# Performance work log

Hardware: AMD Instinct MI355X
Metric: run time of the kernel (lower is better)

## Reference

```python
import jax, jax.numpy as jnp
import numpy as np

NUM_HEADS = 32
NUM_KV_HEADS = 8
HEAD_DIM = 128
PAGE_SIZE = 16
NUM_PAGES = 512
PAGES_PER_SEQ = 256  # 4096 cached tokens
Q_LEN = 1024
SCALE = 0.08838834764831845  # 1/sqrt(HEAD_DIM)


def setup_inputs() -> dict:
    key = jax.random.key(0)
    k1, k2, k3, k4, k5 = jax.random.split(key, 5)
    q = jax.random.normal(k1, (Q_LEN, NUM_HEADS * HEAD_DIM), dtype=jnp.float32)
    k = jax.random.normal(k2, (Q_LEN, NUM_KV_HEADS * HEAD_DIM), dtype=jnp.float32)
    v = jax.random.normal(k3, (Q_LEN, NUM_KV_HEADS * HEAD_DIM), dtype=jnp.float32)
    # paged KV cache: [num_pages, 2 (k/v), num_kv_heads, page_size, head_dim]
    kv_cache = jax.random.normal(
        k4, (NUM_PAGES, 2, NUM_KV_HEADS, PAGE_SIZE, HEAD_DIM), dtype=jnp.float32)
    block_table = jnp.sort(
        jax.random.randint(k5, (PAGES_PER_SEQ,), 0, NUM_PAGES, dtype=jnp.int32))
    return {"q": q, "k": k, "v": v, "kv_cache": kv_cache,
            "block_table": block_table}


def reference(q, k, v, kv_cache, block_table):
    # reshape flat projections into heads
    q = q.reshape(-1, NUM_HEADS, HEAD_DIM)          # [Tq, H, D]
    k = k.reshape(-1, NUM_KV_HEADS, HEAD_DIM)       # [Tq, Hkv, D]
    v = v.reshape(-1, NUM_KV_HEADS, HEAD_DIM)

    # gather paged KV cache into continuous tensors (all pages full)
    pages = kv_cache[block_table]                   # [P, 2, Hkv, ps, D]
    # per-page [Hkv, ps, D] -> [ps, Hkv, D], then concat along token dim
    past = jnp.transpose(pages, (1, 0, 3, 2, 4))    # [2, P, ps, Hkv, D]
    past = past.reshape(2, -1, NUM_KV_HEADS, HEAD_DIM)
    past_k, past_v = past[0], past[1]               # [Tpast, Hkv, D]

    k_full = jnp.concatenate([past_k, k], axis=0)   # [Tkv, Hkv, D]
    v_full = jnp.concatenate([past_v, v], axis=0)

    # GQA: repeat kv heads to match query heads
    heads_per_kv = NUM_HEADS // NUM_KV_HEADS
    k_full = jnp.repeat(k_full, heads_per_kv, axis=1)  # [Tkv, H, D]
    v_full = jnp.repeat(v_full, heads_per_kv, axis=1)

    qh = jnp.transpose(q, (1, 0, 2))                # [H, Tq, D]
    kh = jnp.transpose(k_full, (1, 0, 2))           # [H, Tkv, D]
    vh = jnp.transpose(v_full, (1, 0, 2))

    scores = jnp.einsum('hqd,hkd->hqk', qh, kh) * SCALE  # [H, Tq, Tkv]

    # prefill causal mask exactly as in the source: triu(ones(q_len, kv_len), 1)
    q_len, kv_len = qh.shape[1], kh.shape[1]
    causal = jnp.triu(jnp.ones((q_len, kv_len), dtype=bool), k=1)
    scores = jnp.where(causal[None, :, :], -jnp.inf, scores)

    attn = jax.nn.softmax(scores.astype(jnp.float32), axis=-1).astype(qh.dtype)
    out = jnp.einsum('hqk,hkd->hqd', attn, vh)      # [H, Tq, D]
    out = jnp.transpose(out, (1, 0, 2)).reshape(-1, NUM_HEADS * HEAD_DIM)
    return out
```

## Files before the change

kernel.cpp:

```cpp
#include <hip/hip_runtime.h>
#include <hip/hip_bf16.h>


#define NUM_HEADS 32
#define HEAD_DIM 128
#define Q_STRIDE 4096
#define SCALE 0.08838834764831845f
#define RESCALE_THR 8.0f
#define KSW_TILE 16384
#define VSW_OFF (2 * 1024 * 1024)

typedef short short8 __attribute__((ext_vector_type(8)));
typedef float f32x4 __attribute__((ext_vector_type(4)));
typedef unsigned short ushort_t;
typedef unsigned int uint_t;

__device__ __forceinline__ ushort_t f2bf(float f) {
    return __builtin_bit_cast(ushort_t, __float2bfloat16(f));
}
__device__ __forceinline__ uint_t pk2(float a, float b) {
    return (uint_t)f2bf(a) | ((uint_t)f2bf(b) << 16);
}

__launch_bounds__(256)
__global__ void prep_kv(const float* __restrict__ kvc,
                        const int* __restrict__ bt,
                        char* __restrict__ wsb)
{
    __shared__ float sVt[64 * 128];
    const int blk = blockIdx.x;
    const int hkv = blk >> 4;
    const int jb  = blk & 15;
    const int tid = threadIdx.x;
    char* kout = wsb + (size_t)(hkv * 16 + jb) * KSW_TILE;
    char* vout = wsb + VSW_OFF + (size_t)(hkv * 16 + jb) * KSW_TILE;

#pragma unroll
    for (int i = 0; i < 4; ++i) {
        const int u = tid + i * 256;
        const int t = u >> 4, c = u & 15;
        const int gtok = jb * 64 + t;
        const int page = bt[gtok >> 4];
        const float* src = kvc + (size_t)page * 32768 + (size_t)hkv * 2048
                         + (gtok & 15) * 128 + c * 8;
        float4 a = *(const float4*)src;
        float4 b = *(const float4*)(src + 4);
        uint4 p;
        p.x = pk2(a.x, a.y); p.y = pk2(a.z, a.w);
        p.z = pk2(b.x, b.y); p.w = pk2(b.z, b.w);
        *(uint4*)(kout + t * 256 + ((c * 16) ^ ((t & 7) << 4))) = p;
    }
#pragma unroll
    for (int i = 0; i < 8; ++i) {
        const int u = tid + i * 256;
        const int t = u >> 5, c4 = u & 31;
        const int gtok = jb * 64 + t;
        const int page = bt[gtok >> 4];
        const float* src = kvc + (size_t)page * 32768 + 16384
                         + (size_t)hkv * 2048 + (gtok & 15) * 128 + c4 * 4;
        *(float4*)(sVt + t * 128 + c4 * 4) = *(const float4*)src;
    }
    __syncthreads();
#pragma unroll
    for (int i = 0; i < 4; ++i) {
        const int u = tid + i * 256;
        const int d = u >> 3, ch = u & 7;
        float v[8];
#pragma unroll
        for (int k = 0; k < 8; ++k) v[k] = sVt[(8 * ch + k) * 128 + d];
        uint4 p;
        p.x = pk2(v[0], v[1]); p.y = pk2(v[2], v[3]);
        p.z = pk2(v[4], v[5]); p.w = pk2(v[6], v[7]);
        *(uint4*)(vout + ((d * 128 + 16 * ch) ^ ((d & 7) << 4))) = p;
    }
}

#define GLL16(G, L) __builtin_amdgcn_global_load_lds(                         \
    (const uint_t __attribute__((address_space(1)))*)(G),                     \
    (uint_t __attribute__((address_space(3)))*)(L), 16, 0, 0)

#define STAGE(JB, KB, VB) {                                                   \
    const char* ks = kvbf + (size_t)(hkv * 16 + (JB)) * KSW_TILE              \
                   + w * 4096 + lane * 16;                                    \
    const char* vs = ks + VSW_OFF;                                            \
    _Pragma("unroll")                                                         \
    for (int i = 0; i < 4; ++i) {                                             \
        GLL16(ks + i * 1024, (KB) + w * 4096 + i * 1024);                     \
        GLL16(vs + i * 1024, (VB) + w * 4096 + i * 1024);                     \
    }                                                                         \
}

__launch_bounds__(256)
__global__ void attn_main(const float* __restrict__ q,
                          const char* __restrict__ kvbf,
                          float* __restrict__ out)
{
    __shared__ __align__(16) char sK[2][16384];
    __shared__ __align__(16) char sV[2][16384];
    __shared__ __align__(16) char sP[4][2048];

    const int bid = blockIdx.x;
    const int h   = bid & 31;
    const int qt  = 15 - (bid >> 5);
    const int hkv = h >> 2;
    const int tid  = threadIdx.x;
    const int w    = tid >> 6;
    const int lane = tid & 63;
    const int l15  = lane & 15;
    const int lhi  = lane >> 4;

    short8 qf[4];
    {
        const int qrow = qt * 64 + w * 16 + l15;
        const float* qp = q + (size_t)qrow * Q_STRIDE + h * HEAD_DIM;
#pragma unroll
        for (int s = 0; s < 4; ++s) {
            const int d0 = s * 32 + lhi * 8;
            float4 a = *(const float4*)(qp + d0);
            float4 b = *(const float4*)(qp + d0 + 4);
            short8 v;
            v[0] = (short)f2bf(a.x * SCALE); v[1] = (short)f2bf(a.y * SCALE);
            v[2] = (short)f2bf(a.z * SCALE); v[3] = (short)f2bf(a.w * SCALE);
            v[4] = (short)f2bf(b.x * SCALE); v[5] = (short)f2bf(b.y * SCALE);
            v[6] = (short)f2bf(b.z * SCALE); v[7] = (short)f2bf(b.w * SCALE);
            qf[s] = v;
        }
    }

    f32x4 acc[8];
#pragma unroll
    for (int n2 = 0; n2 < 8; ++n2) acc[n2] = (f32x4){0.f, 0.f, 0.f, 0.f};
    float m_run[4]  = {-1e30f, -1e30f, -1e30f, -1e30f};
    float l_part[4] = {0.f, 0.f, 0.f, 0.f};

    STAGE(0, sK[0], sV[0])
    __syncthreads();

    for (int jb = 0; jb <= qt; ++jb) {
        const int cur = jb & 1;
        char* kbuf = sK[cur];
        char* vbuf = sV[cur];
        const bool pf = (jb < qt);
        if (pf) {
            STAGE(jb + 1, sK[cur ^ 1], sV[cur ^ 1])
        }

        f32x4 sacc[4];
#pragma unroll
        for (int n = 0; n < 4; ++n) sacc[n] = (f32x4){0.f, 0.f, 0.f, 0.f};
#pragma unroll
        for (int s = 0; s < 4; ++s) {
#pragma unroll
            for (int n = 0; n < 4; ++n) {
                const int tok = n * 16 + l15;
                const uint_t byte = (uint_t)(tok * 256)
                    + (((uint_t)((s * 32 + lhi * 8) * 2)) ^ ((uint_t)((tok & 7) << 4)));
                short8 kb = *(const short8*)(kbuf + byte);
                sacc[n] = __builtin_amdgcn_mfma_f32_16x16x32_bf16(qf[s], kb, sacc[n], 0, 0, 0);
            }
        }

        const bool diag = (jb == qt);
        float pv[4][4];
#pragma unroll
        for (int n = 0; n < 4; ++n)
#pragma unroll
            for (int j = 0; j < 4; ++j) {
                float x = sacc[n][j];
                if (diag) {
                    const int tok = jb * 64 + n * 16 + l15;
                    const int qg  = qt * 64 + w * 16 + lhi * 4 + j;
                    if (tok > qg) x = -1e30f;
                }
                pv[n][j] = x;
            }
#pragma unroll
        for (int j = 0; j < 4; ++j) {
            float lmax = fmaxf(fmaxf(pv[0][j], pv[1][j]), fmaxf(pv[2][j], pv[3][j]));
            if (__any(lmax > m_run[j] + RESCALE_THR)) {
                float mt = lmax;
#pragma unroll
                for (int off = 1; off < 16; off <<= 1)
                    mt = fmaxf(mt, __shfl_xor(mt, off));
                const float mn = fmaxf(m_run[j], mt);
                const float alpha = __expf(m_run[j] - mn);
                m_run[j] = mn;
                l_part[j] *= alpha;
#pragma unroll
                for (int n2 = 0; n2 < 8; ++n2) acc[n2][j] *= alpha;
            }
            float ls = 0.f;
#pragma unroll
            for (int n = 0; n < 4; ++n) {
                float p = __expf(pv[n][j] - m_run[j]);
                pv[n][j] = p;
                ls += p;
            }
            l_part[j] += ls;
        }

        char* pb = sP[w];
#pragma unroll
        for (int n = 0; n < 4; ++n)
#pragma unroll
            for (int j = 0; j < 4; ++j) {
                const int r = lhi * 4 + j;
                const uint_t byte = (uint_t)(r * 128)
                    + (((uint_t)((n * 16 + l15) * 2)) ^ ((uint_t)((r & 7) << 4)));
                *(ushort_t*)(pb + byte) = f2bf(pv[n][j]);
            }

#pragma unroll
        for (int s2 = 0; s2 < 2; ++s2) {
            const uint_t pbyte = (uint_t)(l15 * 128)
                + (((uint_t)((s2 * 32 + lhi * 8) * 2)) ^ ((uint_t)((l15 & 7) << 4)));
            short8 pa = *(const short8*)(pb + pbyte);
#pragma unroll
            for (int n2 = 0; n2 < 8; ++n2) {
                const int dim = n2 * 16 + l15;
                const uint_t vbyte = (uint_t)(dim * 128)
                    + (((uint_t)((s2 * 32 + lhi * 8) * 2)) ^ ((uint_t)((dim & 7) << 4)));
                short8 vbf = *(const short8*)(vbuf + vbyte);
                acc[n2] = __builtin_amdgcn_mfma_f32_16x16x32_bf16(pa, vbf, acc[n2], 0, 0, 0);
            }
        }

        if (pf) __syncthreads();
    }

#pragma unroll
    for (int j = 0; j < 4; ++j) {
        float lsum = l_part[j];
#pragma unroll
        for (int off = 1; off < 16; off <<= 1)
            lsum += __shfl_xor(lsum, off);
        const float inv = 1.0f / lsum;
        const int qg = qt * 64 + w * 16 + lhi * 4 + j;
        float* dst = out + (size_t)qg * Q_STRIDE + h * HEAD_DIM;
#pragma unroll
        for (int n2 = 0; n2 < 8; ++n2)
            dst[n2 * 16 + l15] = acc[n2][j] * inv;
    }
}

extern "C" void kernel_launch(void* const* d_in, const int* in_sizes, int n_in,
                              void* d_out, int out_size, void* d_ws, size_t ws_size,
                              hipStream_t stream) {
    const float* q   = (const float*)d_in[0];
    const float* kvc = (const float*)d_in[3];
    const int*   bt  = (const int*)d_in[4];
    float* out = (float*)d_out;
    char*  wsb = (char*)d_ws;
    prep_kv<<<dim3(128), dim3(256), 0, stream>>>(kvc, bt, wsb);
    attn_main<<<dim3(512), dim3(256), 0, stream>>>(q, wsb, out);
}
```

Measured before the change: 45.80 us.

## Process two query heads per block with 32 rows per wave to reuse K/V

```diff
diff --git a/kernel.cpp b/kernel.cpp
--- a/kernel.cpp
+++ b/kernel.cpp
@@ -97,21 +97,24 @@
 {
     __shared__ __align__(16) char sK[2][16384];
     __shared__ __align__(16) char sV[2][16384];
-    __shared__ __align__(16) char sP[4][2048];
+    __shared__ __align__(16) char sP[4][2][2048];
 
     const int bid = blockIdx.x;
-    const int h   = bid & 31;
-    const int qt  = 15 - (bid >> 5);
-    const int hkv = h >> 2;
+    const int hp  = bid & 15;
+    const int qt  = 15 - (bid >> 4);
+    const int hkv = hp >> 1;
     const int tid  = threadIdx.x;
     const int w    = tid >> 6;
     const int lane = tid & 63;
     const int l15  = lane & 15;
     const int lhi  = lane >> 4;
-
-    short8 qf[4];
-    {
-        const int qrow = qt * 64 + w * 16 + l15;
+    const int h    = hp * 2 + (w >> 1);
+    const int rh   = w & 1;
+
+    short8 qf[2][4];
+#pragma unroll
+    for (int rt = 0; rt < 2; ++rt) {
+        const int qrow = qt * 64 + rh * 32 + rt * 16 + l15;
         const float* qp = q + (size_t)qrow * Q_STRIDE + h * HEAD_DIM;
 #pragma unroll
         for (int s = 0; s < 4; ++s) {
@@ -123,15 +126,17 @@
             v[2] = (short)f2bf(a.z * SCALE); v[3] = (short)f2bf(a.w * SCALE);
             v[4] = (short)f2bf(b.x * SCALE); v[5] = (short)f2bf(b.y * SCALE);
             v[6] = (short)f2bf(b.z * SCALE); v[7] = (short)f2bf(b.w * SCALE);
-            qf[s] = v;
-        }
-    }
-
-    f32x4 acc[8];
-#pragma unroll
-    for (int n2 = 0; n2 < 8; ++n2) acc[n2] = (f32x4){0.f, 0.f, 0.f, 0.f};
-    float m_run[4]  = {-1e30f, -1e30f, -1e30f, -1e30f};
-    float l_part[4] = {0.f, 0.f, 0.f, 0.f};
+            qf[rt][s] = v;
+        }
+    }
+
+    f32x4 acc[2][8];
+#pragma unroll
+    for (int rt = 0; rt < 2; ++rt)
+#pragma unroll
+        for (int n2 = 0; n2 < 8; ++n2) acc[rt][n2] = (f32x4){0.f, 0.f, 0.f, 0.f};
+    float m_run[2][4]  = {{-1e30f,-1e30f,-1e30f,-1e30f},{-1e30f,-1e30f,-1e30f,-1e30f}};
+    float l_part[2][4] = {{0.f,0.f,0.f,0.f},{0.f,0.f,0.f,0.f}};
 
     STAGE(0, sK[0], sV[0])
     __syncthreads();
@@ -145,9 +150,11 @@
             STAGE(jb + 1, sK[cur ^ 1], sV[cur ^ 1])
         }
 
-        f32x4 sacc[4];
-#pragma unroll
-        for (int n = 0; n < 4; ++n) sacc[n] = (f32x4){0.f, 0.f, 0.f, 0.f};
+        f32x4 sacc[2][4];
+#pragma unroll
+        for (int rt = 0; rt < 2; ++rt)
+#pragma unroll
+            for (int n = 0; n < 4; ++n) sacc[rt][n] = (f32x4){0.f, 0.f, 0.f, 0.f};
 #pragma unroll
         for (int s = 0; s < 4; ++s) {
 #pragma unroll
@@ -156,72 +163,76 @@
                 const uint_t byte = (uint_t)(tok * 256)
                     + (((uint_t)((s * 32 + lhi * 8) * 2)) ^ ((uint_t)((tok & 7) << 4)));
                 short8 kb = *(const short8*)(kbuf + byte);
-                sacc[n] = __builtin_amdgcn_mfma_f32_16x16x32_bf16(qf[s], kb, sacc[n], 0, 0, 0);
+                sacc[0][n] = __builtin_amdgcn_mfma_f32_16x16x32_bf16(qf[0][s], kb, sacc[0][n], 0, 0, 0);
+                sacc[1][n] = __builtin_amdgcn_mfma_f32_16x16x32_bf16(qf[1][s], kb, sacc[1][n], 0, 0, 0);
             }
         }
 
         const bool diag = (jb == qt);
-        float pv[4][4];
-#pragma unroll
-        for (int n = 0; n < 4; ++n)
+#pragma unroll
+        for (int rt = 0; rt < 2; ++rt) {
+            if (diag) {
+#pragma unroll
+                for (int n = 0; n < 4; ++n)
+#pragma unroll
+                    for (int j = 0; j < 4; ++j) {
+                        const int tok = jb * 64 + n * 16 + l15;
+                        const int qg  = qt * 64 + rh * 32 + rt * 16 + lhi * 4 + j;
+                        if (tok > qg) sacc[rt][n][j] = -1e30f;
+                    }
+            }
 #pragma unroll
             for (int j = 0; j < 4; ++j) {
-                float x = sacc[n][j];
-                if (diag) {
-                    const int tok = jb * 64 + n * 16 + l15;
-                    const int qg  = qt * 64 + w * 16 + lhi * 4 + j;
-                    if (tok > qg) x = -1e30f;
+                float lmax = fmaxf(fmaxf(sacc[rt][0][j], sacc[rt][1][j]),
+                                   fmaxf(sacc[rt][2][j], sacc[rt][3][j]));
+                if (__any(lmax > m_run[rt][j] + RESCALE_THR)) {
+                    float mt = lmax;
+#pragma unroll
+                    for (int off = 1; off < 16; off <<= 1)
+                        mt = fmaxf(mt, __shfl_xor(mt, off));
+                    const float mn = fmaxf(m_run[rt][j], mt);
+                    const float alpha = __expf(m_run[rt][j] - mn);
+                    m_run[rt][j] = mn;
+                    l_part[rt][j] *= alpha;
+#pragma unroll
+                    for (int n2 = 0; n2 < 8; ++n2) acc[rt][n2][j] *= alpha;
                 }
-                pv[n][j] = x;
-            }
-#pragma unroll
-        for (int j = 0; j < 4; ++j) {
-            float lmax = fmaxf(fmaxf(pv[0][j], pv[1][j]), fmaxf(pv[2][j], pv[3][j]));
-            if (__any(lmax > m_run[j] + RESCALE_THR)) {
-                float mt = lmax;
-#pragma unroll
-                for (int off = 1; off < 16; off <<= 1)
-                    mt = fmaxf(mt, __shfl_xor(mt, off));
-                const float mn = fmaxf(m_run[j], mt);
-                const float alpha = __expf(m_run[j] - mn);
-                m_run[j] = mn;
-                l_part[j] *= alpha;
-#pragma unroll
-                for (int n2 = 0; n2 < 8; ++n2) acc[n2][j] *= alpha;
-            }
-            float ls = 0.f;
-#pragma unroll
-            for (int n = 0; n < 4; ++n) {
-                float p = __expf(pv[n][j] - m_run[j]);
-                pv[n][j] = p;
-                ls += p;
-            }
-            l_part[j] += ls;
-        }
-
-        char* pb = sP[w];
-#pragma unroll
-        for (int n = 0; n < 4; ++n)
-#pragma unroll
-            for (int j = 0; j < 4; ++j) {
-                const int r = lhi * 4 + j;
-                const uint_t byte = (uint_t)(r * 128)
-                    + (((uint_t)((n * 16 + l15) * 2)) ^ ((uint_t)((r & 7) << 4)));
-                *(ushort_t*)(pb + byte) = f2bf(pv[n][j]);
-            }
+                float ls = 0.f;
+#pragma unroll
+                for (int n = 0; n < 4; ++n) {
+                    float p = __expf(sacc[rt][n][j] - m_run[rt][j]);
+                    sacc[rt][n][j] = p;
+                    ls += p;
+                }
+                l_part[rt][j] += ls;
+            }
+
+            char* pb = sP[w][rt];
+#pragma unroll
+            for (int n = 0; n < 4; ++n)
+#pragma unroll
+                for (int j = 0; j < 4; ++j) {
+                    const int r = lhi * 4 + j;
+                    const uint_t byte = (uint_t)(r * 128)
+                        + (((uint_t)((n * 16 + l15) * 2)) ^ ((uint_t)((r & 7) << 4)));
+                    *(ushort_t*)(pb + byte) = f2bf(sacc[rt][n][j]);
+                }
+        }
 
 #pragma unroll
         for (int s2 = 0; s2 < 2; ++s2) {
             const uint_t pbyte = (uint_t)(l15 * 128)
                 + (((uint_t)((s2 * 32 + lhi * 8) * 2)) ^ ((uint_t)((l15 & 7) << 4)));
-            short8 pa = *(const short8*)(pb + pbyte);
+            short8 pa0 = *(const short8*)(sP[w][0] + pbyte);
+            short8 pa1 = *(const short8*)(sP[w][1] + pbyte);
 #pragma unroll
             for (int n2 = 0; n2 < 8; ++n2) {
                 const int dim = n2 * 16 + l15;
                 const uint_t vbyte = (uint_t)(dim * 128)
                     + (((uint_t)((s2 * 32 + lhi * 8) * 2)) ^ ((uint_t)((dim & 7) << 4)));
                 short8 vbf = *(const short8*)(vbuf + vbyte);
-                acc[n2] = __builtin_amdgcn_mfma_f32_16x16x32_bf16(pa, vbf, acc[n2], 0, 0, 0);
+                acc[0][n2] = __builtin_amdgcn_mfma_f32_16x16x32_bf16(pa0, vbf, acc[0][n2], 0, 0, 0);
+                acc[1][n2] = __builtin_amdgcn_mfma_f32_16x16x32_bf16(pa1, vbf, acc[1][n2], 0, 0, 0);
             }
         }
 
@@ -229,17 +240,19 @@
     }
 
 #pragma unroll
+    for (int rt = 0; rt < 2; ++rt)
+#pragma unroll
     for (int j = 0; j < 4; ++j) {
-        float lsum = l_part[j];
+        float lsum = l_part[rt][j];
 #pragma unroll
         for (int off = 1; off < 16; off <<= 1)
             lsum += __shfl_xor(lsum, off);
         const float inv = 1.0f / lsum;
-        const int qg = qt * 64 + w * 16 + lhi * 4 + j;
+        const int qg = qt * 64 + rh * 32 + rt * 16 + lhi * 4 + j;
         float* dst = out + (size_t)qg * Q_STRIDE + h * HEAD_DIM;
 #pragma unroll
         for (int n2 = 0; n2 < 8; ++n2)
-            dst[n2 * 16 + l15] = acc[n2][j] * inv;
+            dst[n2 * 16 + l15] = acc[rt][n2][j] * inv;
     }
 }
 
@@ -252,5 +265,5 @@
     float* out = (float*)d_out;
     char*  wsb = (char*)d_ws;
     prep_kv<<<dim3(128), dim3(256), 0, stream>>>(kvc, bt, wsb);
-    attn_main<<<dim3(512), dim3(256), 0, stream>>>(q, wsb, out);
-}
+    attn_main<<<dim3(256), dim3(256), 0, stream>>>(q, wsb, out);
+}
```

Result: slower. 56.90 us (+24.3%).

## Split KV range across two blocks and pair GQA heads per block

Applied to the files above, without the earlier changes.

```diff
diff --git a/kernel.cpp b/kernel.cpp
--- a/kernel.cpp
+++ b/kernel.cpp
@@ -2,13 +2,14 @@
 #include <hip/hip_bf16.h>
 
 
-#define NUM_HEADS 32
-#define HEAD_DIM 128
 #define Q_STRIDE 4096
 #define SCALE 0.08838834764831845f
 #define RESCALE_THR 8.0f
 #define KSW_TILE 16384
-#define VSW_OFF (2 * 1024 * 1024)
+#define VSW_OFF  (2 * 1024 * 1024)
+#define ACC1_OFF (4 * 1024 * 1024)
+#define ML0_OFF  (ACC1_OFF + 32768 * 256)
+#define ML1_OFF  (ML0_OFF + 32768 * 8)
 
 typedef short short8 __attribute__((ext_vector_type(8)));
 typedef float f32x4 __attribute__((ext_vector_type(4)));
@@ -20,6 +21,10 @@
 }
 __device__ __forceinline__ uint_t pk2(float a, float b) {
     return (uint_t)f2bf(a) | ((uint_t)f2bf(b) << 16);
+}
+__device__ __forceinline__ float bf2f(ushort_t u) {
+    uint_t x = ((uint_t)u) << 16;
+    return __builtin_bit_cast(float, x);
 }
 
 __launch_bounds__(256)
@@ -80,39 +85,47 @@
     (uint_t __attribute__((address_space(3)))*)(L), 16, 0, 0)
 
 #define STAGE(JB, KB, VB) {                                                   \
-    const char* ks = kvbf + (size_t)(hkv * 16 + (JB)) * KSW_TILE              \
-                   + w * 4096 + lane * 16;                                    \
-    const char* vs = ks + VSW_OFF;                                            \
-    _Pragma("unroll")                                                         \
-    for (int i = 0; i < 4; ++i) {                                             \
-        GLL16(ks + i * 1024, (KB) + w * 4096 + i * 1024);                     \
-        GLL16(vs + i * 1024, (VB) + w * 4096 + i * 1024);                     \
-    }                                                                         \
-}
-
-__launch_bounds__(256)
+    const char* b_ = kvbf + (size_t)(hkv * 16 + (JB)) * KSW_TILE              \
+                   + w * 1024 + lane * 16;                                    \
+    GLL16(b_,                  (KB) + w * 1024);                              \
+    GLL16(b_ + 8192,           (KB) + w * 1024 + 8192);                       \
+    GLL16(b_ + VSW_OFF,        (VB) + w * 1024);                              \
+    GLL16(b_ + VSW_OFF + 8192, (VB) + w * 1024 + 8192);                       \
+}
+
+__launch_bounds__(512)
 __global__ void attn_main(const float* __restrict__ q,
                           const char* __restrict__ kvbf,
-                          float* __restrict__ out)
+                          float* __restrict__ out,
+                          char* __restrict__ wsb)
 {
     __shared__ __align__(16) char sK[2][16384];
     __shared__ __align__(16) char sV[2][16384];
-    __shared__ __align__(16) char sP[4][2048];
-
-    const int bid = blockIdx.x;
-    const int h   = bid & 31;
-    const int qt  = 15 - (bid >> 5);
-    const int hkv = h >> 2;
+    __shared__ __align__(16) char sP[8][2048];
+
+    const int bid  = blockIdx.x;
+    const int half = bid >> 8;
+    const int rr   = bid & 255;
+    const int g    = rr >> 4;
+    const int hp   = rr & 15;
+    const int qt   = half ? g : (15 - g);
+    const int nt   = qt + 1;
+    const int nt0  = (nt + 1) >> 1;
+    const int jb0  = half ? nt0 : 0;
+    const int jb1  = half ? nt  : nt0;
+    const int hkv  = hp >> 1;
     const int tid  = threadIdx.x;
     const int w    = tid >> 6;
     const int lane = tid & 63;
     const int l15  = lane & 15;
     const int lhi  = lane >> 4;
+    const int h    = hp * 2 + (w >> 2);
+    const int rg   = w & 3;
 
     short8 qf[4];
     {
-        const int qrow = qt * 64 + w * 16 + l15;
-        const float* qp = q + (size_t)qrow * Q_STRIDE + h * HEAD_DIM;
+        const int qrow = qt * 64 + rg * 16 + l15;
+        const float* qp = q + (size_t)qrow * Q_STRIDE + h * 128;
 #pragma unroll
         for (int s = 0; s < 4; ++s) {
             const int d0 = s * 32 + lhi * 8;
@@ -133,14 +146,16 @@
     float m_run[4]  = {-1e30f, -1e30f, -1e30f, -1e30f};
     float l_part[4] = {0.f, 0.f, 0.f, 0.f};
 
-    STAGE(0, sK[0], sV[0])
+    if (jb0 < jb1) {
+        STAGE(jb0, sK[0], sV[0])
+    }
     __syncthreads();
 
-    for (int jb = 0; jb <= qt; ++jb) {
-        const int cur = jb & 1;
+    for (int jb = jb0; jb < jb1; ++jb) {
+        const int cur = (jb - jb0) & 1;
         char* kbuf = sK[cur];
         char* vbuf = sV[cur];
-        const bool pf = (jb < qt);
+        const bool pf = (jb + 1 < jb1);
         if (pf) {
             STAGE(jb + 1, sK[cur ^ 1], sV[cur ^ 1])
         }
@@ -161,22 +176,20 @@
         }
 
         const bool diag = (jb == qt);
-        float pv[4][4];
-#pragma unroll
-        for (int n = 0; n < 4; ++n)
-#pragma unroll
-            for (int j = 0; j < 4; ++j) {
-                float x = sacc[n][j];
-                if (diag) {
+        if (diag) {
+#pragma unroll
+            for (int n = 0; n < 4; ++n)
+#pragma unroll
+                for (int j = 0; j < 4; ++j) {
                     const int tok = jb * 64 + n * 16 + l15;
-                    const int qg  = qt * 64 + w * 16 + lhi * 4 + j;
-                    if (tok > qg) x = -1e30f;
+                    const int qg  = qt * 64 + rg * 16 + lhi * 4 + j;
+                    if (tok > qg) sacc[n][j] = -1e30f;
                 }
-                pv[n][j] = x;
-            }
+        }
 #pragma unroll
         for (int j = 0; j < 4; ++j) {
-            float lmax = fmaxf(fmaxf(pv[0][j], pv[1][j]), fmaxf(pv[2][j], pv[3][j]));
+            float lmax = fmaxf(fmaxf(sacc[0][j], sacc[1][j]),
+                               fmaxf(sacc[2][j], sacc[3][j]));
             if (__any(lmax > m_run[j] + RESCALE_THR)) {
                 float mt = lmax;
 #pragma unroll
@@ -192,8 +205,8 @@
             float ls = 0.f;
 #pragma unroll
             for (int n = 0; n < 4; ++n) {
-                float p = __expf(pv[n][j] - m_run[j]);
-                pv[n][j] = p;
+                float p = __expf(sacc[n][j] - m_run[j]);
+                sacc[n][j] = p;
                 ls += p;
             }
             l_part[j] += ls;
@@ -207,7 +220,7 @@
                 const int r = lhi * 4 + j;
                 const uint_t byte = (uint_t)(r * 128)
                     + (((uint_t)((n * 16 + l15) * 2)) ^ ((uint_t)((r & 7) << 4)));
-                *(ushort_t*)(pb + byte) = f2bf(pv[n][j]);
+                *(ushort_t*)(pb + byte) = f2bf(sacc[n][j]);
             }
 
 #pragma unroll
@@ -234,12 +247,60 @@
 #pragma unroll
         for (int off = 1; off < 16; off <<= 1)
             lsum += __shfl_xor(lsum, off);
-        const float inv = 1.0f / lsum;
-        const int qg = qt * 64 + w * 16 + lhi * 4 + j;
-        float* dst = out + (size_t)qg * Q_STRIDE + h * HEAD_DIM;
-#pragma unroll
-        for (int n2 = 0; n2 < 8; ++n2)
-            dst[n2 * 16 + l15] = acc[n2][j] * inv;
+        const int row64 = rg * 16 + lhi * 4 + j;
+        const int qg    = qt * 64 + row64;
+        const int idx   = (qt * 32 + h) * 64 + row64;
+        if (half == 0) {
+            float* dst = out + (size_t)qg * Q_STRIDE + h * 128;
+#pragma unroll
+            for (int n2 = 0; n2 < 8; ++n2)
+                dst[n2 * 16 + l15] = acc[n2][j];
+            if (l15 == 0) {
+                float* ml = (float*)(wsb + ML0_OFF) + (size_t)idx * 2;
+                ml[0] = m_run[j]; ml[1] = lsum;
+            }
+        } else {
+            ushort_t* dst = (ushort_t*)(wsb + ACC1_OFF) + (size_t)idx * 128;
+#pragma unroll
+            for (int n2 = 0; n2 < 8; ++n2)
+                dst[n2 * 16 + l15] = f2bf(acc[n2][j]);
+            if (l15 == 0) {
+                float* ml = (float*)(wsb + ML1_OFF) + (size_t)idx * 2;
+                ml[0] = m_run[j]; ml[1] = lsum;
+            }
+        }
+    }
+}
+
+__launch_bounds__(256)
+__global__ void attn_combine(float* __restrict__ out, const char* __restrict__ wsb)
+{
+    const int pid = blockIdx.x;
+    const int qt = pid >> 5;
+    const int h  = pid & 31;
+    const int tid = threadIdx.x;
+    const int d4  = (tid & 31) * 4;
+    const float* ml0b = (const float*)(wsb + ML0_OFF);
+    const float* ml1b = (const float*)(wsb + ML1_OFF);
+    const ushort_t* a1b = (const ushort_t*)(wsb + ACC1_OFF);
+
+#pragma unroll
+    for (int p = 0; p < 8; ++p) {
+        const int r = (tid >> 5) + p * 8;
+        const size_t idx = (size_t)pid * 64 + r;
+        const float m1 = ml0b[idx * 2], l1 = ml0b[idx * 2 + 1];
+        const float m2 = ml1b[idx * 2], l2 = ml1b[idx * 2 + 1];
+        const float m  = fmaxf(m1, m2);
+        const float a1 = __expf(m1 - m), a2 = __expf(m2 - m);
+        const float inv = 1.0f / (l1 * a1 + l2 * a2);
+        float* o = out + (size_t)(qt * 64 + r) * Q_STRIDE + h * 128 + d4;
+        const ushort_t* y4 = a1b + idx * 128 + d4;
+        float4 x = *(const float4*)o;
+        x.x = (x.x * a1 + bf2f(y4[0]) * a2) * inv;
+        x.y = (x.y * a1 + bf2f(y4[1]) * a2) * inv;
+        x.z = (x.z * a1 + bf2f(y4[2]) * a2) * inv;
+        x.w = (x.w * a1 + bf2f(y4[3]) * a2) * inv;
+        *(float4*)o = x;
     }
 }
 
@@ -252,5 +313,6 @@
     float* out = (float*)d_out;
     char*  wsb = (char*)d_ws;
     prep_kv<<<dim3(128), dim3(256), 0, stream>>>(kvc, bt, wsb);
-    attn_main<<<dim3(512), dim3(256), 0, stream>>>(q, wsb, out);
-}
+    attn_main<<<dim3(512), dim3(512), 0, stream>>>(q, wsb, out, wsb);
+    attn_combine<<<dim3(512), dim3(256), 0, stream>>>(out, wsb);
+}
```

Result: slower. 54.37 us (+18.7%).

## Load K/V fragments directly from global into registers, drop LDS staging

Applied to the files above, without the earlier changes.

```diff
diff --git a/kernel.cpp b/kernel.cpp
--- a/kernel.cpp
+++ b/kernel.cpp
@@ -2,8 +2,6 @@
 #include <hip/hip_bf16.h>
 
 
-#define NUM_HEADS 32
-#define HEAD_DIM 128
 #define Q_STRIDE 4096
 #define SCALE 0.08838834764831845f
 #define RESCALE_THR 8.0f
@@ -48,7 +46,7 @@
         uint4 p;
         p.x = pk2(a.x, a.y); p.y = pk2(a.z, a.w);
         p.z = pk2(b.x, b.y); p.w = pk2(b.z, b.w);
-        *(uint4*)(kout + t * 256 + ((c * 16) ^ ((t & 7) << 4))) = p;
+        *(uint4*)(kout + t * 256 + c * 16) = p;
     }
 #pragma unroll
     for (int i = 0; i < 8; ++i) {
@@ -71,23 +69,8 @@
         uint4 p;
         p.x = pk2(v[0], v[1]); p.y = pk2(v[2], v[3]);
         p.z = pk2(v[4], v[5]); p.w = pk2(v[6], v[7]);
-        *(uint4*)(vout + ((d * 128 + 16 * ch) ^ ((d & 7) << 4))) = p;
-    }
-}
-
-#define GLL16(G, L) __builtin_amdgcn_global_load_lds(                         \
-    (const uint_t __attribute__((address_space(1)))*)(G),                     \
-    (uint_t __attribute__((address_space(3)))*)(L), 16, 0, 0)
-
-#define STAGE(JB, KB, VB) {                                                   \
-    const char* ks = kvbf + (size_t)(hkv * 16 + (JB)) * KSW_TILE              \
-                   + w * 4096 + lane * 16;                                    \
-    const char* vs = ks + VSW_OFF;                                            \
-    _Pragma("unroll")                                                         \
-    for (int i = 0; i < 4; ++i) {                                             \
-        GLL16(ks + i * 1024, (KB) + w * 4096 + i * 1024);                     \
-        GLL16(vs + i * 1024, (VB) + w * 4096 + i * 1024);                     \
-    }                                                                         \
+        *(uint4*)(vout + d * 128 + 16 * ch) = p;
+    }
 }
 
 __launch_bounds__(256)
@@ -95,24 +78,23 @@
                           const char* __restrict__ kvbf,
                           float* __restrict__ out)
 {
-    __shared__ __align__(16) char sK[2][16384];
-    __shared__ __align__(16) char sV[2][16384];
     __shared__ __align__(16) char sP[4][2048];
 
     const int bid = blockIdx.x;
-    const int h   = bid & 31;
     const int qt  = 15 - (bid >> 5);
-    const int hkv = h >> 2;
+    const int hkv = (bid >> 2) & 7;
+    const int rg  = bid & 3;
     const int tid  = threadIdx.x;
     const int w    = tid >> 6;
     const int lane = tid & 63;
     const int l15  = lane & 15;
     const int lhi  = lane >> 4;
+    const int h    = hkv * 4 + w;
 
     short8 qf[4];
     {
-        const int qrow = qt * 64 + w * 16 + l15;
-        const float* qp = q + (size_t)qrow * Q_STRIDE + h * HEAD_DIM;
+        const int qrow = qt * 64 + rg * 16 + l15;
+        const float* qp = q + (size_t)qrow * Q_STRIDE + h * 128;
 #pragma unroll
         for (int s = 0; s < 4; ++s) {
             const int d0 = s * 32 + lhi * 8;
@@ -133,50 +115,52 @@
     float m_run[4]  = {-1e30f, -1e30f, -1e30f, -1e30f};
     float l_part[4] = {0.f, 0.f, 0.f, 0.f};
 
-    STAGE(0, sK[0], sV[0])
-    __syncthreads();
+    char* pb = sP[w];
+    const int kfb = (l15 * 256) + (lhi * 16);
+    const int vfb = (l15 * 128) + (lhi * 16);
 
     for (int jb = 0; jb <= qt; ++jb) {
-        const int cur = jb & 1;
-        char* kbuf = sK[cur];
-        char* vbuf = sV[cur];
-        const bool pf = (jb < qt);
-        if (pf) {
-            STAGE(jb + 1, sK[cur ^ 1], sV[cur ^ 1])
-        }
+        const char* kt = kvbf + (size_t)(hkv * 16 + jb) * KSW_TILE;
+        const char* vt = kt + VSW_OFF;
+
+        short8 kb[4][4];
+#pragma unroll
+        for (int s = 0; s < 4; ++s)
+#pragma unroll
+            for (int n = 0; n < 4; ++n)
+                kb[s][n] = *(const short8*)(kt + kfb + n * 4096 + s * 64);
 
         f32x4 sacc[4];
 #pragma unroll
         for (int n = 0; n < 4; ++n) sacc[n] = (f32x4){0.f, 0.f, 0.f, 0.f};
 #pragma unroll
-        for (int s = 0; s < 4; ++s) {
-#pragma unroll
-            for (int n = 0; n < 4; ++n) {
-                const int tok = n * 16 + l15;
-                const uint_t byte = (uint_t)(tok * 256)
-                    + (((uint_t)((s * 32 + lhi * 8) * 2)) ^ ((uint_t)((tok & 7) << 4)));
-                short8 kb = *(const short8*)(kbuf + byte);
-                sacc[n] = __builtin_amdgcn_mfma_f32_16x16x32_bf16(qf[s], kb, sacc[n], 0, 0, 0);
-            }
-        }
+        for (int s = 0; s < 4; ++s)
+#pragma unroll
+            for (int n = 0; n < 4; ++n)
+                sacc[n] = __builtin_amdgcn_mfma_f32_16x16x32_bf16(qf[s], kb[s][n], sacc[n], 0, 0, 0);
+
+        short8 vb[2][8];
+#pragma unroll
+        for (int s2 = 0; s2 < 2; ++s2)
+#pragma unroll
+            for (int n2 = 0; n2 < 8; ++n2)
+                vb[s2][n2] = *(const short8*)(vt + vfb + n2 * 2048 + s2 * 64);
 
         const bool diag = (jb == qt);
-        float pv[4][4];
-#pragma unroll
-        for (int n = 0; n < 4; ++n)
-#pragma unroll
-            for (int j = 0; j < 4; ++j) {
-                float x = sacc[n][j];
-                if (diag) {
+        if (diag) {
+#pragma unroll
+            for (int n = 0; n < 4; ++n)
+#pragma unroll
+                for (int j = 0; j < 4; ++j) {
                     const int tok = jb * 64 + n * 16 + l15;
-                    const int qg  = qt * 64 + w * 16 + lhi * 4 + j;
-                    if (tok > qg) x = -1e30f;
+                    const int qg  = qt * 64 + rg * 16 + lhi * 4 + j;
+                    if (tok > qg) sacc[n][j] = -1e30f;
                 }
-                pv[n][j] = x;
-            }
+        }
 #pragma unroll
         for (int j = 0; j < 4; ++j) {
-            float lmax = fmaxf(fmaxf(pv[0][j], pv[1][j]), fmaxf(pv[2][j], pv[3][j]));
+            float lmax = fmaxf(fmaxf(sacc[0][j], sacc[1][j]),
+                               fmaxf(sacc[2][j], sacc[3][j]));
             if (__any(lmax > m_run[j] + RESCALE_THR)) {
                 float mt = lmax;
 #pragma unroll
@@ -192,14 +176,13 @@
             float ls = 0.f;
 #pragma unroll
             for (int n = 0; n < 4; ++n) {
-                float p = __expf(pv[n][j] - m_run[j]);
-                pv[n][j] = p;
+                float p = __expf(sacc[n][j] - m_run[j]);
+                sacc[n][j] = p;
                 ls += p;
             }
             l_part[j] += ls;
         }
 
-        char* pb = sP[w];
 #pragma unroll
         for (int n = 0; n < 4; ++n)
 #pragma unroll
@@ -207,7 +190,7 @@
                 const int r = lhi * 4 + j;
                 const uint_t byte = (uint_t)(r * 128)
                     + (((uint_t)((n * 16 + l15) * 2)) ^ ((uint_t)((r & 7) << 4)));
-                *(ushort_t*)(pb + byte) = f2bf(pv[n][j]);
+                *(ushort_t*)(pb + byte) = f2bf(sacc[n][j]);
             }
 
 #pragma unroll
@@ -216,16 +199,9 @@
                 + (((uint_t)((s2 * 32 + lhi * 8) * 2)) ^ ((uint_t)((l15 & 7) << 4)));
             short8 pa = *(const short8*)(pb + pbyte);
 #pragma unroll
-            for (int n2 = 0; n2 < 8; ++n2) {
-                const int dim = n2 * 16 + l15;
-                const uint_t vbyte = (uint_t)(dim * 128)
-                    + (((uint_t)((s2 * 32 + lhi * 8) * 2)) ^ ((uint_t)((dim & 7) << 4)));
-                short8 vbf = *(const short8*)(vbuf + vbyte);
-                acc[n2] = __builtin_amdgcn_mfma_f32_16x16x32_bf16(pa, vbf, acc[n2], 0, 0, 0);
-            }
-        }
-
-        if (pf) __syncthreads();
+            for (int n2 = 0; n2 < 8; ++n2)
+                acc[n2] = __builtin_amdgcn_mfma_f32_16x16x32_bf16(pa, vb[s2][n2], acc[n2], 0, 0, 0);
+        }
     }
 
 #pragma unroll
@@ -235,8 +211,8 @@
         for (int off = 1; off < 16; off <<= 1)
             lsum += __shfl_xor(lsum, off);
         const float inv = 1.0f / lsum;
-        const int qg = qt * 64 + w * 16 + lhi * 4 + j;
-        float* dst = out + (size_t)qg * Q_STRIDE + h * HEAD_DIM;
+        const int qg = qt * 64 + rg * 16 + lhi * 4 + j;
+        float* dst = out + (size_t)qg * Q_STRIDE + h * 128;
 #pragma unroll
         for (int n2 = 0; n2 < 8; ++n2)
             dst[n2 * 16 + l15] = acc[n2][j] * inv;
```

Result: slower. 101.3 us (+121.2%).
